# Kernel optimization log

Hardware: AMD Instinct MI355X
Metric: run time of the kernel (lower is better)

The kernel has to match this reference:

```python
import math
import jax, jax.numpy as jnp
import numpy as np

H, W = 512, 512            # volume_shape
N_ANGLES = 360
N_DET = 736                # num_detectors
DET_SPACING = 1.0          # detector_spacing (voxel units)
STEP = 1.0                 # ray-marching step (voxel units)
N_STEPS = int(math.ceil(math.hypot(H, W)))  # 725 samples along each ray


def setup_inputs() -> dict:
    key = jax.random.key(0)
    k1, k2 = jax.random.split(key)
    x = jax.random.normal(k1, (H, W), dtype=jnp.float32)
    # learned reconstruction parameter (zeros in the module; small randn here so the add is non-trivial)
    reco = jax.random.normal(k2, (H, W), dtype=jnp.float32) * 0.1
    angles = jnp.linspace(0.0, np.pi, N_ANGLES, endpoint=False, dtype=jnp.float32)
    return {"x": x, "reco": reco, "angles": angles}


def _bilinear(img, xs, ys):
    """Bilinear interpolation of img[y, x] with zero padding outside."""
    h, w = img.shape
    x0 = jnp.floor(xs)
    y0 = jnp.floor(ys)
    wx = xs - x0
    wy = ys - y0
    x0i = x0.astype(jnp.int32)
    y0i = y0.astype(jnp.int32)

    def fetch(yi, xi):
        inb = (xi >= 0) & (xi < w) & (yi >= 0) & (yi < h)
        v = img[jnp.clip(yi, 0, h - 1), jnp.clip(xi, 0, w - 1)]
        return jnp.where(inb, v, jnp.zeros((), img.dtype))

    return (fetch(y0i, x0i) * (1 - wx) * (1 - wy)
            + fetch(y0i, x0i + 1) * wx * (1 - wy)
            + fetch(y0i + 1, x0i) * (1 - wx) * wy
            + fetch(y0i + 1, x0i + 1) * wx * wy)


def _radon(img, angles):
    """Parallel-beam ray-driven forward projection -> sinogram (n_angles, n_det)."""
    cx = (W - 1) * 0.5
    cy = (H - 1) * 0.5
    u = (jnp.arange(N_DET, dtype=img.dtype) - (N_DET - 1) * 0.5) * DET_SPACING
    t = (jnp.arange(N_STEPS, dtype=img.dtype) - (N_STEPS - 1) * 0.5) * STEP

    def one_angle(theta):
        c = jnp.cos(theta)
        s = jnp.sin(theta)
        # ray: p(t) = u * perp + t * dir, dir = (c, s), perp = (-s, c); centered on volume
        xs = -s * u[:, None] + c * t[None, :] + cx   # (D, T)
        ys = c * u[:, None] + s * t[None, :] + cy    # (D, T)
        return _bilinear(img, xs, ys).sum(axis=1) * STEP  # (D,)

    # lax.map keeps per-angle intermediates small (ray-driven accumulation)
    return jax.lax.map(one_angle, angles)  # (A, D)


def reference(x, reco, angles):
    updated_reco = x + reco
    current_sino = _radon(updated_reco, angles)
    return current_sino, updated_reco
```

## Files before the change

### kernel.cpp

```cpp
#include <hip/hip_runtime.h>
#include <math.h>

constexpr int H = 512, W = 512;
constexpr int N_ANGLES = 360;
constexpr int N_DET = 736;
constexpr int N_STEPS = 725;
constexpr int SINO_SIZE = N_ANGLES * N_DET;

constexpr int DET_TILE = 64;
constexpr int K_TILE   = 64;
constexpr int PITCH    = 100;
constexpr int ROWS     = 93;
constexpr int QCHUNKS  = PITCH / 4;
constexpr int MAXJ     = 5;

constexpr int PADX = 96, PADY = 96;
constexpr int PW = 720;
constexpr int PH = 704;
constexpr size_t PAD_BYTES = (size_t)PW * PH * 4;

typedef float v2f __attribute__((ext_vector_type(2)));
typedef __fp16 h2f __attribute__((ext_vector_type(2)));
union PackU { unsigned u; h2f h; };

__global__ void pad_kernel(const float* __restrict__ x,
                           const float* __restrict__ reco,
                           unsigned* __restrict__ padded2,
                           float* __restrict__ updated) {
    int i = blockIdx.x * blockDim.x + threadIdx.x;
    if (i >= PW * PH) return;
    int p = i / PW, q = i - p * PW;
    int gy = p - PADY, gx = q - PADX;
    float v0 = 0.0f, v1 = 0.0f;
    if ((unsigned)gx < (unsigned)W) {
        if ((unsigned)gy < (unsigned)H) {
            int gi = gy * W + gx;
            v0 = x[gi] + reco[gi];
            updated[gi] = v0;
        }
        if ((unsigned)(gy + 1) < (unsigned)H) {
            int gi = (gy + 1) * W + gx;
            v1 = x[gi] + reco[gi];
        }
    }
    PackU pk;
    pk.h = __builtin_amdgcn_cvt_pkrtz(v0, v1);
    padded2[i] = pk.u;
}

__global__ void add_kernel(const float4* __restrict__ x,
                           const float4* __restrict__ reco,
                           float4* __restrict__ out) {
    int i = blockIdx.x * blockDim.x + threadIdx.x;
    float4 a = x[i];
    float4 b = reco[i];
    out[i] = make_float4(a.x + b.x, a.y + b.y, a.z + b.z, a.w + b.w);
}

template <bool DMA>
__global__ __launch_bounds__(512, 8) void radon_kernel(const void* __restrict__ imgv,
                                                       const float* __restrict__ angles,
                                                       float* __restrict__ sino) {
    __shared__ unsigned tile[ROWS * PITCH];

    const int tid = threadIdx.x;
    const int w   = tid >> 6;
    const int l   = tid & 63;
    const int dt_ = 16 * (w & 3) + (l & 15);
    const int klr = 4 * (w >> 2) + (l >> 4);
    const int a   = blockIdx.y;
    const int d0  = blockIdx.x * DET_TILE;

    const float theta = angles[a];
    const float c = cosf(theta);
    const float s = sinf(theta);
    const float ac = fabsf(c), as = fabsf(s);
    const float cx = (W - 1) * 0.5f;
    const float cy = (H - 1) * 0.5f;
    const float t_off = (N_STEPS - 1) * 0.5f;

    const float u   = (float)(d0 + dt_) - (N_DET - 1) * 0.5f;
    const float bxu = cx - s * u;
    const float byu = cy + c * u;

    const float uLo = (float)d0 - (N_DET - 1) * 0.5f;
    const float uHi = uLo + (DET_TILE - 1);
    float su0 = s * uLo, su1 = s * uHi;
    float smin = fminf(su0, su1), smax = fmaxf(su0, su1);
    float cu0 = c * uLo, cu1 = c * uHi;
    float cmin = fminf(cu0, cu1), cmax = fmaxf(cu0, cu1);

    float tmin = -1e30f, tmax = 1e30f;
    {
        float xlo = -1.0f - cx + smin;
        float xhi = (float)W - cx + smax;
        if (ac > 1e-12f) {
            float t0 = xlo / c, t1 = xhi / c;
            tmin = fmaxf(tmin, fminf(t0, t1));
            tmax = fminf(tmax, fmaxf(t0, t1));
        } else if (xlo > 0.0f || xhi < 0.0f) {
            tmax = -2e30f;
        }
    }
    {
        float ylo = -1.0f - cy - cmax;
        float yhi = (float)H - cy - cmin;
        if (as > 1e-12f) {
            float t0 = ylo / s, t1 = yhi / s;
            tmin = fmaxf(tmin, fminf(t0, t1));
            tmax = fminf(tmax, fmaxf(t0, t1));
        } else if (ylo > 0.0f || yhi < 0.0f) {
            tmax = -2e30f;
        }
    }
    const int kminU = (int)fminf(725.0f, fmaxf(0.0f, ceilf(tmin + t_off) - 1.0f));
    const int kmaxU = (int)fmaxf(-1.0f, fminf((float)(N_STEPS - 1), floorf(tmax + t_off) + 1.0f));

    const float ucf = uLo + 0.5f * (DET_TILE - 1);
    const v2f dinc = {8.0f * c, 8.0f * s};

    float acc = 0.0f;

    for (int k0 = kminU; k0 <= kmaxU; k0 += K_TILE) {
        const int k1 = min(k0 + K_TILE - 1, kmaxU);
        const float t0f = (float)k0 - t_off;
        const float dt  = (float)(k1 - k0);
        const float tc  = t0f + 0.5f * dt;
        const float xc_ = fmaf(c, tc, cx) - s * ucf;
        const float yc_ = fmaf(s, tc, cy) + c * ucf;
        const float hx = fmaf(0.5f * ac, dt, 0.5f * (DET_TILE - 1) * as) + 0.5f;
        const float hy = fmaf(0.5f * as, dt, 0.5f * (DET_TILE - 1) * ac) + 0.5f;
        const int x0 = ((int)floorf(xc_ - hx)) & ~3;
        const int y0 = (int)floorf(yc_ - hy);
        const int bh = min((int)floorf(yc_ + hy) + 1 - y0, ROWS);

        if constexpr (DMA) {
            const unsigned* img2 = (const unsigned*)imgv;
            const int total = bh * QCHUNKS;
            const unsigned* srow = img2 + (size_t)(y0 + PADY) * PW + (x0 + PADX);
            #pragma unroll
            for (int j = 0; j < MAXJ; ++j) {
                const int i = tid + j * 512;
                if (i < total) {
                    const int r  = i / QCHUNKS;
                    const int ch = i - r * QCHUNKS;
                    const unsigned* src = srow + r * PW + ch * 4;
                    unsigned* dst = tile + (size_t)(i & ~63) * 4;
                    __builtin_amdgcn_global_load_lds(
                        (const __attribute__((address_space(1))) unsigned*)src,
                        (__attribute__((address_space(3))) unsigned*)dst,
                        16, 0, 0);
                }
            }
        } else {
            const float* img = (const float*)imgv;
            const int total = bh * PITCH;
            for (int i = tid; i < total; i += 512) {
                int r  = i / PITCH;
                int gxx = i - r * PITCH + x0;
                int gy = y0 + r;
                float v0 = 0.0f, v1 = 0.0f;
                if ((unsigned)gxx < (unsigned)W) {
                    if ((unsigned)gy < (unsigned)H)       v0 = img[gy * W + gxx];
                    if ((unsigned)(gy + 1) < (unsigned)H) v1 = img[(gy + 1) * W + gxx];
                }
                PackU pk;
                pk.h = __builtin_amdgcn_cvt_pkrtz(v0, v1);
                tile[i] = pk.u;
            }
        }
        __syncthreads();

        const int kst = k0 + klr;
        v2f pos = {fmaf(c, (float)kst - t_off, bxu) - (float)x0,
                   fmaf(s, (float)kst - t_off, byu) - (float)y0};
        #pragma unroll 4
        for (int k = kst; k <= k1; k += 8) {
            int xi = (int)pos.x;
            int yi = (int)pos.y;
            float wx = __builtin_amdgcn_fractf(pos.x);
            float wy = __builtin_amdgcn_fractf(pos.y);
            int idx = __mul24(yi, PITCH) + xi;
            PackU q0, q1;
            q0.u = tile[idx];
            q1.u = tile[idx + 1];
            v2f c0 = {(float)q0.h.x, (float)q0.h.y};
            v2f c1 = {(float)q1.h.x, (float)q1.h.y};
            v2f diff = c1 - c0;
            v2f wx2 = {wx, wx};
            v2f tb = __builtin_elementwise_fma(wx2, diff, c0);
            acc = fmaf(wy, tb.y - tb.x, acc + tb.x);
            pos += dinc;
        }
        __syncthreads();
    }

    acc += __shfl_xor(acc, 16);
    acc += __shfl_xor(acc, 32);
    float* scratch = (float*)tile;
    if (l < 16) scratch[w * 16 + l] = acc;
    __syncthreads();
    if (tid < DET_TILE) {
        int g  = tid >> 4;
        int dd = tid & 15;
        float r = scratch[g * 16 + dd] + scratch[(g + 4) * 16 + dd];
        int dglob = d0 + tid;
        if (dglob < N_DET) sino[a * N_DET + dglob] = r;
    }
}

extern "C" void kernel_launch(void* const* d_in, const int* in_sizes, int n_in,
                              void* d_out, int out_size, void* d_ws, size_t ws_size,
                              hipStream_t stream) {
    const float* x      = (const float*)d_in[0];
    const float* reco   = (const float*)d_in[1];
    const float* angles = (const float*)d_in[2];

    float* sino    = (float*)d_out;
    float* updated = (float*)d_out + SINO_SIZE;

    dim3 grid((N_DET + DET_TILE - 1) / DET_TILE, N_ANGLES);

    if (ws_size >= PAD_BYTES) {
        unsigned* padded2 = (unsigned*)d_ws;
        pad_kernel<<<(PW * PH + 255) / 256, 256, 0, stream>>>(x, reco, padded2, updated);
        radon_kernel<true><<<grid, 512, 0, stream>>>(padded2, angles, sino);
    } else {
        int n4 = (H * W) / 4;
        add_kernel<<<n4 / 256, 256, 0, stream>>>(
            (const float4*)x, (const float4*)reco, (float4*)updated);
        radon_kernel<false><<<grid, 512, 0, stream>>>(updated, angles, sino);
    }
}
```

Measured before the change: 99.10 us.

## Double-buffer LDS tile staging to overlap DMA with ray accumulation

The DMA path now stages the next K-tile's image window into a second LDS buffer while the current tile is being sampled. This hides global-to-LDS load latency behind the bilinear accumulation and cuts one barrier per iteration. In exchange, LDS use per block doubles to about 74 KB and the launch-bounds occupancy hint drops from 8 to 4. That roughly halves the number of resident blocks per CU, so there is less latency hiding from wave-level parallelism.

```diff
diff --git a/kernel.cpp b/kernel.cpp
--- a/kernel.cpp
+++ b/kernel.cpp
@@ -13,6 +13,7 @@
 constexpr int ROWS     = 93;
 constexpr int QCHUNKS  = PITCH / 4;
 constexpr int MAXJ     = 5;
+constexpr int TILE_DW  = ROWS * PITCH;
 
 constexpr int PADX = 96, PADY = 96;
 constexpr int PW = 720;
@@ -58,10 +59,10 @@
 }
 
 template <bool DMA>
-__global__ __launch_bounds__(512, 8) void radon_kernel(const void* __restrict__ imgv,
+__global__ __launch_bounds__(512, 4) void radon_kernel(const void* __restrict__ imgv,
                                                        const float* __restrict__ angles,
                                                        float* __restrict__ sino) {
-    __shared__ unsigned tile[ROWS * PITCH];
+    __shared__ unsigned tile[2 * TILE_DW];
 
     const int tid = threadIdx.x;
     const int w   = tid >> 6;
@@ -119,23 +120,25 @@
     const float ucf = uLo + 0.5f * (DET_TILE - 1);
     const v2f dinc = {8.0f * c, 8.0f * s};
 
-    float acc = 0.0f;
-
-    for (int k0 = kminU; k0 <= kmaxU; k0 += K_TILE) {
+    auto bbox = [&](int k0, int& x0, int& y0, int& bh) {
         const int k1 = min(k0 + K_TILE - 1, kmaxU);
         const float t0f = (float)k0 - t_off;
-        const float dt  = (float)(k1 - k0);
-        const float tc  = t0f + 0.5f * dt;
+        const float dtf = (float)(k1 - k0);
+        const float tc  = t0f + 0.5f * dtf;
         const float xc_ = fmaf(c, tc, cx) - s * ucf;
         const float yc_ = fmaf(s, tc, cy) + c * ucf;
-        const float hx = fmaf(0.5f * ac, dt, 0.5f * (DET_TILE - 1) * as) + 0.5f;
-        const float hy = fmaf(0.5f * as, dt, 0.5f * (DET_TILE - 1) * ac) + 0.5f;
-        const int x0 = ((int)floorf(xc_ - hx)) & ~3;
-        const int y0 = (int)floorf(yc_ - hy);
-        const int bh = min((int)floorf(yc_ + hy) + 1 - y0, ROWS);
-
-        if constexpr (DMA) {
-            const unsigned* img2 = (const unsigned*)imgv;
+        const float hx = fmaf(0.5f * ac, dtf, 0.5f * (DET_TILE - 1) * as) + 0.5f;
+        const float hy = fmaf(0.5f * as, dtf, 0.5f * (DET_TILE - 1) * ac) + 0.5f;
+        x0 = ((int)floorf(xc_ - hx)) & ~3;
+        y0 = (int)floorf(yc_ - hy);
+        bh = min((int)floorf(yc_ + hy) + 1 - y0, ROWS);
+    };
+
+    float acc = 0.0f;
+
+    if constexpr (DMA) {
+        const unsigned* img2 = (const unsigned*)imgv;
+        auto stage = [&](unsigned* buf, int x0, int y0, int bh) {
             const int total = bh * QCHUNKS;
             const unsigned* srow = img2 + (size_t)(y0 + PADY) * PW + (x0 + PADX);
             #pragma unroll
@@ -145,15 +148,66 @@
                     const int r  = i / QCHUNKS;
                     const int ch = i - r * QCHUNKS;
                     const unsigned* src = srow + r * PW + ch * 4;
-                    unsigned* dst = tile + (size_t)(i & ~63) * 4;
+                    unsigned* dst = buf + (i & ~63) * 4;
                     __builtin_amdgcn_global_load_lds(
                         (const __attribute__((address_space(1))) unsigned*)src,
                         (__attribute__((address_space(3))) unsigned*)dst,
                         16, 0, 0);
                 }
             }
-        } else {
-            const float* img = (const float*)imgv;
+        };
+
+        unsigned* bcur = tile;
+        unsigned* bnxt = tile + TILE_DW;
+
+        if (kminU <= kmaxU) {
+            int x0, y0, bh;
+            bbox(kminU, x0, y0, bh);
+            stage(bcur, x0, y0, bh);
+            __syncthreads();
+
+            for (int k0 = kminU; k0 <= kmaxU; k0 += K_TILE) {
+                const int k1 = min(k0 + K_TILE - 1, kmaxU);
+
+                int nx0 = 0, ny0 = 0, nbh = 0;
+                if (k0 + K_TILE <= kmaxU) {
+                    bbox(k0 + K_TILE, nx0, ny0, nbh);
+                    stage(bnxt, nx0, ny0, nbh);
+                }
+
+                const int kst = k0 + klr;
+                v2f pos = {fmaf(c, (float)kst - t_off, bxu) - (float)x0,
+                           fmaf(s, (float)kst - t_off, byu) - (float)y0};
+                #pragma unroll 4
+                for (int k = kst; k <= k1; k += 8) {
+                    int xi = (int)pos.x;
+                    int yi = (int)pos.y;
+                    float wx = __builtin_amdgcn_fractf(pos.x);
+                    float wy = __builtin_amdgcn_fractf(pos.y);
+                    int idx = __mul24(yi, PITCH) + xi;
+                    PackU q0, q1;
+                    q0.u = bcur[idx];
+                    q1.u = bcur[idx + 1];
+                    v2f c0 = {(float)q0.h.x, (float)q0.h.y};
+                    v2f c1 = {(float)q1.h.x, (float)q1.h.y};
+                    v2f diff = c1 - c0;
+                    v2f wx2 = {wx, wx};
+                    v2f tb = __builtin_elementwise_fma(wx2, diff, c0);
+                    acc = fmaf(wy, tb.y - tb.x, acc + tb.x);
+                    pos += dinc;
+                }
+
+                __syncthreads();
+                x0 = nx0; y0 = ny0;
+                unsigned* tmp = bcur; bcur = bnxt; bnxt = tmp;
+            }
+        }
+    } else {
+        const float* img = (const float*)imgv;
+        for (int k0 = kminU; k0 <= kmaxU; k0 += K_TILE) {
+            const int k1 = min(k0 + K_TILE - 1, kmaxU);
+            int x0, y0, bh;
+            bbox(k0, x0, y0, bh);
             const int total = bh * PITCH;
             for (int i = tid; i < total; i += 512) {
                 int r  = i / PITCH;
@@ -168,31 +222,31 @@
                 pk.h = __builtin_amdgcn_cvt_pkrtz(v0, v1);
                 tile[i] = pk.u;
             }
-        }
-        __syncthreads();
-
-        const int kst = k0 + klr;
-        v2f pos = {fmaf(c, (float)kst - t_off, bxu) - (float)x0,
-                   fmaf(s, (float)kst - t_off, byu) - (float)y0};
-        #pragma unroll 4
-        for (int k = kst; k <= k1; k += 8) {
-            int xi = (int)pos.x;
-            int yi = (int)pos.y;
-            float wx = __builtin_amdgcn_fractf(pos.x);
-            float wy = __builtin_amdgcn_fractf(pos.y);
-            int idx = __mul24(yi, PITCH) + xi;
-            PackU q0, q1;
-            q0.u = tile[idx];
-            q1.u = tile[idx + 1];
-            v2f c0 = {(float)q0.h.x, (float)q0.h.y};
-            v2f c1 = {(float)q1.h.x, (float)q1.h.y};
-            v2f diff = c1 - c0;
-            v2f wx2 = {wx, wx};
-            v2f tb = __builtin_elementwise_fma(wx2, diff, c0);
-            acc = fmaf(wy, tb.y - tb.x, acc + tb.x);
-            pos += dinc;
-        }
-        __syncthreads();
+            __syncthreads();
+
+            const int kst = k0 + klr;
+            v2f pos = {fmaf(c, (float)kst - t_off, bxu) - (float)x0,
+                       fmaf(s, (float)kst - t_off, byu) - (float)y0};
+            #pragma unroll 4
+            for (int k = kst; k <= k1; k += 8) {
+                int xi = (int)pos.x;
+                int yi = (int)pos.y;
+                float wx = __builtin_amdgcn_fractf(pos.x);
+                float wy = __builtin_amdgcn_fractf(pos.y);
+                int idx = __mul24(yi, PITCH) + xi;
+                PackU q0, q1;
+                q0.u = tile[idx];
+                q1.u = tile[idx + 1];
+                v2f c0 = {(float)q0.h.x, (float)q0.h.y};
+                v2f c1 = {(float)q1.h.x, (float)q1.h.y};
+                v2f diff = c1 - c0;
+                v2f wx2 = {wx, wx};
+                v2f tb = __builtin_elementwise_fma(wx2, diff, c0);
+                acc = fmaf(wy, tb.y - tb.x, acc + tb.x);
+                pos += dinc;
+            }
+            __syncthreads();
+        }
     }
 
     acc += __shfl_xor(acc, 16);
```

Result: slower. 118.9 us (+20.0%).
